# Kernel optimization log

Hardware: AMD Instinct MI355X
Metric: run time of the kernel (lower is better)

The kernel has to match this reference:

```python
import jax, jax.numpy as jnp
import numpy as np

B, T, F = 32, 512, 4096
H = 128            # num_lstm
NUM_CLASSES = 2    # dense outputs = NUM_CLASSES + 1 (CTC blank)


def setup_inputs() -> dict:
    key = jax.random.key(0)
    ks = jax.random.split(key, 6)
    x = jax.random.normal(ks[0], (B, T, F), dtype=jnp.float32)
    # Keras LSTM params: kernel [F, 4H], recurrent_kernel [H, 4H], bias [4H]
    # (gate order i, f, c, o). Glorot-ish scaling for stability.
    Wk = jax.random.normal(ks[1], (F, 4 * H), dtype=jnp.float32) / np.sqrt(F)
    Wr = jax.random.normal(ks[2], (H, 4 * H), dtype=jnp.float32) / np.sqrt(H)
    b = jnp.zeros((4 * H,), dtype=jnp.float32).at[H:2 * H].set(1.0)  # unit_forget_bias
    Wd = jax.random.normal(ks[3], (H, NUM_CLASSES + 1), dtype=jnp.float32) / np.sqrt(H)
    bd = jnp.zeros((NUM_CLASSES + 1,), dtype=jnp.float32)
    return {"x": x, "Wk": Wk, "Wr": Wr, "b": b, "Wd": Wd, "bd": bd}


def _lstm(x, Wk, Wr, b):
    # Precompute input projections for all timesteps (big GEMM once).
    z = jnp.einsum("btf,fg->btg", x, Wk) + b          # [B, T, 4H]
    z = jnp.transpose(z, (1, 0, 2))                    # [T, B, 4H]

    def step(carry, z_t):
        h, c = carry
        g = z_t + h @ Wr                               # [B, 4H]
        i = jax.nn.sigmoid(g[:, 0 * H:1 * H])
        f = jax.nn.sigmoid(g[:, 1 * H:2 * H])
        cc = jnp.tanh(g[:, 2 * H:3 * H])
        o = jax.nn.sigmoid(g[:, 3 * H:4 * H])
        c = f * c + i * cc
        h = o * jnp.tanh(c)
        return (h, c), h

    h0 = jnp.zeros((x.shape[0], H), dtype=x.dtype)
    c0 = jnp.zeros((x.shape[0], H), dtype=x.dtype)
    _, hs = jax.lax.scan(step, (h0, c0), z)            # hs: [T, B, H]
    return jnp.transpose(hs, (1, 0, 2))                # [B, T, H]


def reference(x, Wk, Wr, b, Wd, bd):
    # Inference-mode forward (dropout/recurrent_dropout inactive).
    h = _lstm(x, Wk, Wr, b)                            # [B, T, H]
    return h @ Wd + bd                                 # [B, T, num_classes+1]
```

## Files before the change

kernel.cpp:

```cpp
#include <hip/hip_runtime.h>
#include <hip/hip_bf16.h>
#include <hip/hip_fp16.h>
#include <math.h>

#define B_  32
#define T_  512
#define F_  4096
#define H_  128
#define G4H 512
#define NCLS 3
#define M_  (B_ * T_)
#define KSTEPS 128

typedef _Float16 f16x8 __attribute__((ext_vector_type(8)));
typedef _Float16 f16x4 __attribute__((ext_vector_type(4)));
typedef float    f32x4 __attribute__((ext_vector_type(4)));

__device__ __forceinline__ void gl_lds16(const _Float16* g, _Float16* l) {
    __builtin_amdgcn_global_load_lds(
        (const __attribute__((address_space(1))) void*)(g),
        (__attribute__((address_space(3))) void*)(l), 16, 0, 0);
}

__global__ __launch_bounds__(256) void cvt_wkT(
    const float* __restrict__ Wk, _Float16* __restrict__ btK)
{
    __shared__ float ls[64][65];
    const int k0 = blockIdx.x * 64;
    const int n0 = blockIdx.y * 64;
    const int tid = threadIdx.x;

    {
        int r  = tid >> 4;
        int c4 = (tid & 15) * 4;
        #pragma unroll
        for (int p = 0; p < 4; ++p) {
            float4 v = *reinterpret_cast<const float4*>(
                &Wk[(size_t)(k0 + r + p * 16) * G4H + n0 + c4]);
            ls[r + p * 16][c4 + 0] = v.x;
            ls[r + p * 16][c4 + 1] = v.y;
            ls[r + p * 16][c4 + 2] = v.z;
            ls[r + p * 16][c4 + 3] = v.w;
        }
    }
    __syncthreads();
    {
        int rn = tid >> 2;
        int ck = (tid & 3) * 16;
        f16x8 h0, h1;
        #pragma unroll
        for (int j = 0; j < 8; ++j) {
            h0[j] = (_Float16)ls[ck + j][rn];
            h1[j] = (_Float16)ls[ck + 8 + j][rn];
        }
        const int n    = n0 + rn;
        const int kg   = k0 + ck;
        const int kblk = kg >> 5;
        const int kk   = kg & 31;
        const int g0   = kk >> 3;
        const int sw   = (n >> 1) & 3;
        _Float16* base = btK + (size_t)kblk * (512 * 32) + (size_t)n * 32;
        *reinterpret_cast<f16x8*>(base + ((g0 ^ sw) << 3))       = h0;
        *reinterpret_cast<f16x8*>(base + (((g0 + 1) ^ sw) << 3)) = h1;
    }
}

__global__ __launch_bounds__(256) void cvt_wrT(
    const float* __restrict__ Wr, _Float16* __restrict__ wrT)
{
    __shared__ float ls[64][65];
    const int k0 = blockIdx.x * 64;
    const int n0 = blockIdx.y * 64;
    const int tid = threadIdx.x;
    {
        int r  = tid >> 4;
        int c4 = (tid & 15) * 4;
        #pragma unroll
        for (int p = 0; p < 4; ++p) {
            float4 v = *reinterpret_cast<const float4*>(
                &Wr[(size_t)(k0 + r + p * 16) * G4H + n0 + c4]);
            ls[r + p * 16][c4 + 0] = v.x;
            ls[r + p * 16][c4 + 1] = v.y;
            ls[r + p * 16][c4 + 2] = v.z;
            ls[r + p * 16][c4 + 3] = v.w;
        }
    }
    __syncthreads();
    {
        int rn = tid >> 2;
        int ck = (tid & 3) * 16;
        f16x8 h0, h1;
        #pragma unroll
        for (int j = 0; j < 8; ++j) {
            h0[j] = (_Float16)ls[ck + j][rn];
            h1[j] = (_Float16)ls[ck + 8 + j][rn];
        }
        _Float16* dst = &wrT[(size_t)(n0 + rn) * H_ + k0 + ck];
        *reinterpret_cast<f16x8*>(dst)     = h0;
        *reinterpret_cast<f16x8*>(dst + 8) = h1;
    }
}

__device__ __forceinline__ void lds_barrier() {
    asm volatile("s_waitcnt lgkmcnt(0)" ::: "memory");
    __builtin_amdgcn_s_barrier();
    asm volatile("" ::: "memory");
}

__global__ __launch_bounds__(512, 4) void gemm_fused(
    const float* __restrict__ x, const _Float16* __restrict__ btK,
    const float* __restrict__ bias, float* __restrict__ z)
{
    __shared__ __align__(16) _Float16 As[3][64 * 32];
    __shared__ __align__(16) _Float16 Bs[3][256 * 32];

    const int tid = threadIdx.x;
    const int w   = tid >> 6;
    const int l   = tid & 63;
    const int fr  = l & 15;
    const int q   = l >> 4;

    const int bid   = blockIdx.x;
    const int xcd   = bid & 7;
    const int idx   = bid >> 3;
    const int mt    = xcd * 32 + (idx >> 1);
    const int ntile = idx & 1;
    const int m0    = mt * 64;
    const int n0    = ntile * 256;

    const int ar = tid >> 3;
    const int hc = (tid & 7) * 4;
    const int abyte = ((((hc >> 3) ^ ((ar >> 1) & 3)) << 4) | ((hc << 1) & 15));
    const float* xrow = x + (size_t)(m0 + ar) * F_ + hc;

    #define ISSUE_B(t, buf)                                                   \
    {                                                                         \
        const _Float16* ck_ = btK + (size_t)(t) * (512 * 32) + n0 * 32;       \
        gl_lds16(ck_ + w * 1024 + l * 8,       &Bs[buf][w * 1024]);           \
        gl_lds16(ck_ + w * 1024 + 512 + l * 8, &Bs[buf][w * 1024 + 512]);     \
    }

    #define LOADX(t) (*reinterpret_cast<const float4*>(xrow + (size_t)(t) * 32))

    #define WRITE_A(v, buf)                                                   \
    {                                                                         \
        f16x4 hh; hh[0] = (_Float16)v.x; hh[1] = (_Float16)v.y;               \
        hh[2] = (_Float16)v.z; hh[3] = (_Float16)v.w;                         \
        *reinterpret_cast<f16x4*>(                                            \
            reinterpret_cast<char*>(&As[buf][0]) + ar * 64 + abyte) = hh;     \
    }

    #define COMPUTE(buf)                                                      \
    {                                                                         \
        f16x8 af[4], bf[2];                                                   \
        _Pragma("unroll")                                                     \
        for (int i = 0; i < 4; ++i) {                                         \
            int r   = i * 16 + fr;                                            \
            int off = r * 64 + ((q ^ ((r >> 1) & 3)) << 4);                   \
            af[i] = *reinterpret_cast<const f16x8*>(                          \
                reinterpret_cast<const char*>(&As[buf][0]) + off);            \
        }                                                                     \
        _Pragma("unroll")                                                     \
        for (int j = 0; j < 2; ++j) {                                         \
            int n   = w * 32 + j * 16 + fr;                                   \
            int off = n * 64 + ((q ^ ((n >> 1) & 3)) << 4);                   \
            bf[j] = *reinterpret_cast<const f16x8*>(                          \
                reinterpret_cast<const char*>(&Bs[buf][0]) + off);            \
        }                                                                     \
        _Pragma("unroll")                                                     \
        for (int i = 0; i < 4; ++i)                                           \
            _Pragma("unroll")                                                 \
            for (int j = 0; j < 2; ++j)                                       \
                acc[i][j] = __builtin_amdgcn_mfma_f32_16x16x32_f16(           \
                    af[i], bf[j], acc[i][j], 0, 0, 0);                        \
    }

    f32x4 acc[4][2] = {};
    float4 xvA, xvB;

    ISSUE_B(0, 0) xvA = LOADX(0);
    ISSUE_B(1, 1) xvB = LOADX(1);
    WRITE_A(xvA, 0)
    lds_barrier();

    int b0 = 0, b1 = 1, b2 = 2;
    for (int t = 0; t < KSTEPS; t += 2) {
        if (t + 2 < KSTEPS) { ISSUE_B(t + 2, b2) xvA = LOADX(t + 2); }
        if (t + 1 < KSTEPS) WRITE_A(xvB, b1)
        COMPUTE(b0)
        lds_barrier();
        if (t + 3 < KSTEPS) { ISSUE_B(t + 3, b0) xvB = LOADX(t + 3); }
        if (t + 2 < KSTEPS) WRITE_A(xvA, b2)
        COMPUTE(b1)
        lds_barrier();
        int tmp = b2; b2 = b1; b1 = b0; b0 = tmp;
    }
    #undef ISSUE_B
    #undef LOADX
    #undef WRITE_A
    #undef COMPUTE

    #pragma unroll
    for (int j = 0; j < 2; ++j) {
        const int nn = n0 + w * 32 + j * 16 + fr;
        const int ch = (nn & 127) * 4 + (nn >> 7);
        const float bj = bias[nn];
        #pragma unroll
        for (int i = 0; i < 4; ++i)
            #pragma unroll
            for (int r = 0; r < 4; ++r)
                z[(size_t)(m0 + i * 16 + q * 4 + r) * G4H + ch]
                    = acc[i][j][r] + bj;
    }
}

__device__ __forceinline__ float sig_f(float x) {
    return __builtin_amdgcn_rcpf(
        1.0f + __builtin_amdgcn_exp2f(-1.442695040888963f * x));
}
__device__ __forceinline__ float tanh_f(float x) {
    return 1.0f - 2.0f * __builtin_amdgcn_rcpf(
        1.0f + __builtin_amdgcn_exp2f(2.885390081777927f * x));
}

__global__ __launch_bounds__(512, 2) void lstm_mfma(
    const float* __restrict__ z,
    const _Float16* __restrict__ wrT,
    float* __restrict__ hs)
{
    const int b    = blockIdx.x;
    const int tid  = threadIdx.x;
    const int w    = tid >> 6;
    const int lane = tid & 63;
    const int l15  = lane & 15;
    const int q    = lane >> 4;
    const int jj   = w * 16 + l15;

    __shared__ __align__(16) _Float16 hA[2][128];

    f16x8 bf[4][4];
    #pragma unroll
    for (int g = 0; g < 4; ++g)
        #pragma unroll
        for (int kf = 0; kf < 4; ++kf)
            bf[g][kf] = *reinterpret_cast<const f16x8*>(
                &wrT[(size_t)(g * H_ + jj) * H_ + kf * 32 + q * 8]);

    float cstate = 0.f;
    if (tid < 128) reinterpret_cast<unsigned int*>(hA)[tid] = 0u;

    const float* zrow  = z  + (size_t)b * T_ * G4H + jj * 4;
    float*       hbase = hs + (size_t)b * T_ * H_;

    const f32x4 zero4 = {0.f, 0.f, 0.f, 0.f};

    float4 zP0 = *reinterpret_cast<const float4*>(zrow + (size_t)(0 << 9));
    float4 zP1 = *reinterpret_cast<const float4*>(zrow + (size_t)(1 << 9));
    float4 zP2 = *reinterpret_cast<const float4*>(zrow + (size_t)(2 << 9));
    float4 zP3 = *reinterpret_cast<const float4*>(zrow + (size_t)(3 << 9));

    __syncthreads();

    #define LSTM_STEP(t, CUR, ZZ)                                             \
    {                                                                         \
        f16x8 af0 = *reinterpret_cast<const f16x8*>(&hA[CUR][0 * 32 + q * 8]);\
        f16x8 af1 = *reinterpret_cast<const f16x8*>(&hA[CUR][1 * 32 + q * 8]);\
        f16x8 af2 = *reinterpret_cast<const f16x8*>(&hA[CUR][2 * 32 + q * 8]);\
        f16x8 af3 = *reinterpret_cast<const f16x8*>(&hA[CUR][3 * 32 + q * 8]);\
        float zt0_ = ZZ.x, zt1_ = ZZ.y, zt2_ = ZZ.z, zt3_ = ZZ.w;             \
        ZZ = *reinterpret_cast<const float4*>(                                \
            zrow + (size_t)((((t) + 4) & (T_ - 1)) << 9));                    \
        float gv[4];                                                          \
        _Pragma("unroll")                                                     \
        for (int g = 0; g < 4; ++g) {                                         \
            f32x4 aA = __builtin_amdgcn_mfma_f32_16x16x32_f16(                \
                af0, bf[g][0], zero4, 0, 0, 0);                               \
            aA = __builtin_amdgcn_mfma_f32_16x16x32_f16(                      \
                af1, bf[g][1], aA, 0, 0, 0);                                  \
            f32x4 aB = __builtin_amdgcn_mfma_f32_16x16x32_f16(                \
                af2, bf[g][2], zero4, 0, 0, 0);                               \
            aB = __builtin_amdgcn_mfma_f32_16x16x32_f16(                      \
                af3, bf[g][3], aB, 0, 0, 0);                                  \
            gv[g] = aA[0] + aB[0];                                           \
        }                                                                     \
        float iv = sig_f(gv[0] + zt0_);                                       \
        float fv = sig_f(gv[1] + zt1_);                                       \
        float cc = tanh_f(gv[2] + zt2_);                                      \
        float ov = sig_f(gv[3] + zt3_);                                       \
        cstate = fv * cstate + iv * cc;                                       \
        float h = ov * tanh_f(cstate);                                        \
        if (q == 0) {                                                         \
            hA[CUR ^ 1][jj] = (_Float16)h;                                    \
            hbase[((t) << 7) + jj] = h;                                       \
        }                                                                     \
        lds_barrier();                                                        \
    }

    for (int t = 0; t < T_; t += 4) {
        LSTM_STEP(t,     0, zP0)
        LSTM_STEP(t + 1, 1, zP1)
        LSTM_STEP(t + 2, 0, zP2)
        LSTM_STEP(t + 3, 1, zP3)
    }
    #undef LSTM_STEP
}

__global__ __launch_bounds__(256) void dense_out(
    const float* __restrict__ hs, const float* __restrict__ Wd,
    const float* __restrict__ bd, float* __restrict__ out)
{
    int idx = blockIdx.x * 256 + threadIdx.x;
    if (idx >= B_ * T_ * NCLS) return;
    int cls = idx % NCLS;
    int row = idx / NCLS;
    const float* h = hs + (size_t)row * H_;
    float acc = bd[cls];
    #pragma unroll 8
    for (int k = 0; k < H_; ++k) acc += h[k] * Wd[k * NCLS + cls];
    out[idx] = acc;
}

extern "C" void kernel_launch(void* const* d_in, const int* in_sizes, int n_in,
                              void* d_out, int out_size, void* d_ws, size_t ws_size,
                              hipStream_t stream)
{
    const float* x  = (const float*)d_in[0];
    const float* Wk = (const float*)d_in[1];
    const float* Wr = (const float*)d_in[2];
    const float* b  = (const float*)d_in[3];
    const float* Wd = (const float*)d_in[4];
    const float* bd = (const float*)d_in[5];
    float* out = (float*)d_out;

    float*     z   = (float*)d_ws;
    float*     hs  = z + (size_t)M_ * G4H;
    _Float16*  btK = (_Float16*)(hs + (size_t)M_ * H_);
    _Float16*  wrT = btK + (size_t)G4H * F_;

    cvt_wkT<<<dim3(F_ / 64, G4H / 64), 256, 0, stream>>>(Wk, btK);
    cvt_wrT<<<dim3(H_ / 64, G4H / 64), 256, 0, stream>>>(Wr, wrT);
    gemm_fused<<<512, 512, 0, stream>>>(x, btK, b, z);
    lstm_mfma<<<B_, 512, 0, stream>>>(z, wrT, hs);
    int total = B_ * T_ * NCLS;
    dense_out<<<(total + 255) / 256, 256, 0, stream>>>(hs, Wd, bd, out);
}
```

Baseline: 368.9 us.

## Fuse input GEMM and LSTM recurrence with flag-based per-chunk overlap

Merges the input-projection GEMM and the LSTM recurrence into one persistent launch. The first 32 blocks run the recurrence, one per batch row, and the remaining 512 blocks compute GEMM tiles. Tiles are reordered by batch and time chunk, and each one signals completion through an atomic flag, so the recurrence for a batch row can start as soon as its first 64-step chunk of z is ready. This overlaps the sequential recurrence with the GEMM and removes a kernel boundary. In exchange it relies on spin-waiting with cross-block memory ordering, assumes all blocks become resident without deadlock, and increases LDS use per block, which may lower GEMM occupancy.

```diff
diff --git a/kernel.cpp b/kernel.cpp
--- a/kernel.cpp
+++ b/kernel.cpp
@@ -66,12 +66,14 @@
 }
 
 __global__ __launch_bounds__(256) void cvt_wrT(
-    const float* __restrict__ Wr, _Float16* __restrict__ wrT)
+    const float* __restrict__ Wr, _Float16* __restrict__ wrT,
+    unsigned int* __restrict__ flags)
 {
     __shared__ float ls[64][65];
     const int k0 = blockIdx.x * 64;
     const int n0 = blockIdx.y * 64;
     const int tid = threadIdx.x;
+    if (blockIdx.x == 0 && blockIdx.y == 0) flags[tid] = 0u;
     {
         int r  = tid >> 4;
         int c4 = (tid & 15) * 4;
@@ -107,113 +109,6 @@
     asm volatile("" ::: "memory");
 }
 
-__global__ __launch_bounds__(512, 4) void gemm_fused(
-    const float* __restrict__ x, const _Float16* __restrict__ btK,
-    const float* __restrict__ bias, float* __restrict__ z)
-{
-    __shared__ __align__(16) _Float16 As[3][64 * 32];
-    __shared__ __align__(16) _Float16 Bs[3][256 * 32];
-
-    const int tid = threadIdx.x;
-    const int w   = tid >> 6;
-    const int l   = tid & 63;
-    const int fr  = l & 15;
-    const int q   = l >> 4;
-
-    const int bid   = blockIdx.x;
-    const int xcd   = bid & 7;
-    const int idx   = bid >> 3;
-    const int mt    = xcd * 32 + (idx >> 1);
-    const int ntile = idx & 1;
-    const int m0    = mt * 64;
-    const int n0    = ntile * 256;
-
-    const int ar = tid >> 3;
-    const int hc = (tid & 7) * 4;
-    const int abyte = ((((hc >> 3) ^ ((ar >> 1) & 3)) << 4) | ((hc << 1) & 15));
-    const float* xrow = x + (size_t)(m0 + ar) * F_ + hc;
-
-    #define ISSUE_B(t, buf)                                                   \
-    {                                                                         \
-        const _Float16* ck_ = btK + (size_t)(t) * (512 * 32) + n0 * 32;       \
-        gl_lds16(ck_ + w * 1024 + l * 8,       &Bs[buf][w * 1024]);           \
-        gl_lds16(ck_ + w * 1024 + 512 + l * 8, &Bs[buf][w * 1024 + 512]);     \
-    }
-
-    #define LOADX(t) (*reinterpret_cast<const float4*>(xrow + (size_t)(t) * 32))
-
-    #define WRITE_A(v, buf)                                                   \
-    {                                                                         \
-        f16x4 hh; hh[0] = (_Float16)v.x; hh[1] = (_Float16)v.y;               \
-        hh[2] = (_Float16)v.z; hh[3] = (_Float16)v.w;                         \
-        *reinterpret_cast<f16x4*>(                                            \
-            reinterpret_cast<char*>(&As[buf][0]) + ar * 64 + abyte) = hh;     \
-    }
-
-    #define COMPUTE(buf)                                                      \
-    {                                                                         \
-        f16x8 af[4], bf[2];                                                   \
-        _Pragma("unroll")                                                     \
-        for (int i = 0; i < 4; ++i) {                                         \
-            int r   = i * 16 + fr;                                            \
-            int off = r * 64 + ((q ^ ((r >> 1) & 3)) << 4);                   \
-            af[i] = *reinterpret_cast<const f16x8*>(                          \
-                reinterpret_cast<const char*>(&As[buf][0]) + off);            \
-        }                                                                     \
-        _Pragma("unroll")                                                     \
-        for (int j = 0; j < 2; ++j) {                                         \
-            int n   = w * 32 + j * 16 + fr;                                   \
-            int off = n * 64 + ((q ^ ((n >> 1) & 3)) << 4);                   \
-            bf[j] = *reinterpret_cast<const f16x8*>(                          \
-                reinterpret_cast<const char*>(&Bs[buf][0]) + off);            \
-        }                                                                     \
-        _Pragma("unroll")                                                     \
-        for (int i = 0; i < 4; ++i)                                           \
-            _Pragma("unroll")                                                 \
-            for (int j = 0; j < 2; ++j)                                       \
-                acc[i][j] = __builtin_amdgcn_mfma_f32_16x16x32_f16(           \
-                    af[i], bf[j], acc[i][j], 0, 0, 0);                        \
-    }
-
-    f32x4 acc[4][2] = {};
-    float4 xvA, xvB;
-
-    ISSUE_B(0, 0) xvA = LOADX(0);
-    ISSUE_B(1, 1) xvB = LOADX(1);
-    WRITE_A(xvA, 0)
-    lds_barrier();
-
-    int b0 = 0, b1 = 1, b2 = 2;
-    for (int t = 0; t < KSTEPS; t += 2) {
-        if (t + 2 < KSTEPS) { ISSUE_B(t + 2, b2) xvA = LOADX(t + 2); }
-        if (t + 1 < KSTEPS) WRITE_A(xvB, b1)
-        COMPUTE(b0)
-        lds_barrier();
-        if (t + 3 < KSTEPS) { ISSUE_B(t + 3, b0) xvB = LOADX(t + 3); }
-        if (t + 2 < KSTEPS) WRITE_A(xvA, b2)
-        COMPUTE(b1)
-        lds_barrier();
-        int tmp = b2; b2 = b1; b1 = b0; b0 = tmp;
-    }
-    #undef ISSUE_B
-    #undef LOADX
-    #undef WRITE_A
-    #undef COMPUTE
-
-    #pragma unroll
-    for (int j = 0; j < 2; ++j) {
-        const int nn = n0 + w * 32 + j * 16 + fr;
-        const int ch = (nn & 127) * 4 + (nn >> 7);
-        const float bj = bias[nn];
-        #pragma unroll
-        for (int i = 0; i < 4; ++i)
-            #pragma unroll
-            for (int r = 0; r < 4; ++r)
-                z[(size_t)(m0 + i * 16 + q * 4 + r) * G4H + ch]
-                    = acc[i][j][r] + bj;
-    }
-}
-
 __device__ __forceinline__ float sig_f(float x) {
     return __builtin_amdgcn_rcpf(
         1.0f + __builtin_amdgcn_exp2f(-1.442695040888963f * x));
@@ -223,86 +118,218 @@
         1.0f + __builtin_amdgcn_exp2f(2.885390081777927f * x));
 }
 
-__global__ __launch_bounds__(512, 2) void lstm_mfma(
-    const float* __restrict__ z,
-    const _Float16* __restrict__ wrT,
-    float* __restrict__ hs)
-{
-    const int b    = blockIdx.x;
-    const int tid  = threadIdx.x;
-    const int w    = tid >> 6;
-    const int lane = tid & 63;
-    const int l15  = lane & 15;
-    const int q    = lane >> 4;
-    const int jj   = w * 16 + l15;
-
-    __shared__ __align__(16) _Float16 hA[2][128];
-
-    f16x8 bf[4][4];
-    #pragma unroll
-    for (int g = 0; g < 4; ++g)
-        #pragma unroll
-        for (int kf = 0; kf < 4; ++kf)
-            bf[g][kf] = *reinterpret_cast<const f16x8*>(
-                &wrT[(size_t)(g * H_ + jj) * H_ + kf * 32 + q * 8]);
-
-    float cstate = 0.f;
-    if (tid < 128) reinterpret_cast<unsigned int*>(hA)[tid] = 0u;
-
-    const float* zrow  = z  + (size_t)b * T_ * G4H + jj * 4;
-    float*       hbase = hs + (size_t)b * T_ * H_;
-
-    const f32x4 zero4 = {0.f, 0.f, 0.f, 0.f};
-
-    float4 zP0 = *reinterpret_cast<const float4*>(zrow + (size_t)(0 << 9));
-    float4 zP1 = *reinterpret_cast<const float4*>(zrow + (size_t)(1 << 9));
-    float4 zP2 = *reinterpret_cast<const float4*>(zrow + (size_t)(2 << 9));
-    float4 zP3 = *reinterpret_cast<const float4*>(zrow + (size_t)(3 << 9));
-
-    __syncthreads();
-
-    #define LSTM_STEP(t, CUR, ZZ)                                             \
-    {                                                                         \
-        f16x8 af0 = *reinterpret_cast<const f16x8*>(&hA[CUR][0 * 32 + q * 8]);\
-        f16x8 af1 = *reinterpret_cast<const f16x8*>(&hA[CUR][1 * 32 + q * 8]);\
-        f16x8 af2 = *reinterpret_cast<const f16x8*>(&hA[CUR][2 * 32 + q * 8]);\
-        f16x8 af3 = *reinterpret_cast<const f16x8*>(&hA[CUR][3 * 32 + q * 8]);\
-        float zt0_ = ZZ.x, zt1_ = ZZ.y, zt2_ = ZZ.z, zt3_ = ZZ.w;             \
-        ZZ = *reinterpret_cast<const float4*>(                                \
-            zrow + (size_t)((((t) + 4) & (T_ - 1)) << 9));                    \
-        float gv[4];                                                          \
-        _Pragma("unroll")                                                     \
-        for (int g = 0; g < 4; ++g) {                                         \
-            f32x4 aA = __builtin_amdgcn_mfma_f32_16x16x32_f16(                \
-                af0, bf[g][0], zero4, 0, 0, 0);                               \
-            aA = __builtin_amdgcn_mfma_f32_16x16x32_f16(                      \
-                af1, bf[g][1], aA, 0, 0, 0);                                  \
-            f32x4 aB = __builtin_amdgcn_mfma_f32_16x16x32_f16(                \
-                af2, bf[g][2], zero4, 0, 0, 0);                               \
-            aB = __builtin_amdgcn_mfma_f32_16x16x32_f16(                      \
-                af3, bf[g][3], aB, 0, 0, 0);                                  \
-            gv[g] = aA[0] + aB[0];                                           \
-        }                                                                     \
-        float iv = sig_f(gv[0] + zt0_);                                       \
-        float fv = sig_f(gv[1] + zt1_);                                       \
-        float cc = tanh_f(gv[2] + zt2_);                                      \
-        float ov = sig_f(gv[3] + zt3_);                                       \
-        cstate = fv * cstate + iv * cc;                                       \
-        float h = ov * tanh_f(cstate);                                        \
-        if (q == 0) {                                                         \
-            hA[CUR ^ 1][jj] = (_Float16)h;                                    \
-            hbase[((t) << 7) + jj] = h;                                       \
-        }                                                                     \
-        lds_barrier();                                                        \
-    }
-
-    for (int t = 0; t < T_; t += 4) {
-        LSTM_STEP(t,     0, zP0)
-        LSTM_STEP(t + 1, 1, zP1)
-        LSTM_STEP(t + 2, 0, zP2)
-        LSTM_STEP(t + 3, 1, zP3)
-    }
-    #undef LSTM_STEP
+__device__ __forceinline__ void wait_flag2(unsigned int* f) {
+    while (__hip_atomic_load(f, __ATOMIC_ACQUIRE, __HIP_MEMORY_SCOPE_AGENT) < 2u)
+        __builtin_amdgcn_s_sleep(2);
+}
+
+__global__ __launch_bounds__(512, 2) void fused_gemm_lstm(
+    const float* __restrict__ x, const _Float16* __restrict__ btK,
+    const float* __restrict__ bias, float* __restrict__ z,
+    const _Float16* __restrict__ wrT, float* __restrict__ hs,
+    unsigned int* __restrict__ flags)
+{
+    __shared__ __align__(16) char smem[61440];
+    const int bid = blockIdx.x;
+    const int tid = threadIdx.x;
+
+    if (bid >= B_) {
+        char* AsB = smem;
+        char* BsB = smem + 12288;
+
+        const int w   = tid >> 6;
+        const int l   = tid & 63;
+        const int fr  = l & 15;
+        const int q   = l >> 4;
+
+        const int gbid  = bid - B_;
+        const int s     = gbid >> 6;
+        const int i6    = gbid & 63;
+        const int xx    = i6 & 7;
+        const int yy    = (i6 >> 4) & 3;
+        const int ntile = (i6 >> 3) & 1;
+        const int bb    = xx * 4 + yy;
+        const int m0    = bb * T_ + s * 64;
+        const int n0    = ntile * 256;
+
+        const int ar = tid >> 3;
+        const int hc = (tid & 7) * 4;
+        const int abyte = ((((hc >> 3) ^ ((ar >> 1) & 3)) << 4) | ((hc << 1) & 15));
+        const float* xrow = x + (size_t)(m0 + ar) * F_ + hc;
+
+        #define ISSUE_B(t, buf)                                               \
+        {                                                                     \
+            const _Float16* ck_ = btK + (size_t)(t) * (512 * 32) + n0 * 32;   \
+            _Float16* bb_ = (_Float16*)(BsB + (buf) * 16384) + w * 1024;      \
+            gl_lds16(ck_ + w * 1024 + l * 8,       bb_);                      \
+            gl_lds16(ck_ + w * 1024 + 512 + l * 8, bb_ + 512);                \
+        }
+
+        #define LOADX(t) (*reinterpret_cast<const float4*>(xrow + (size_t)(t) * 32))
+
+        #define WRITE_A(v, buf)                                               \
+        {                                                                     \
+            f16x4 hh; hh[0] = (_Float16)v.x; hh[1] = (_Float16)v.y;           \
+            hh[2] = (_Float16)v.z; hh[3] = (_Float16)v.w;                     \
+            *reinterpret_cast<f16x4*>(                                        \
+                AsB + (buf) * 4096 + ar * 64 + abyte) = hh;                   \
+        }
+
+        #define COMPUTE(buf)                                                  \
+        {                                                                     \
+            f16x8 af[4], bf[2];                                               \
+            _Pragma("unroll")                                                 \
+            for (int i = 0; i < 4; ++i) {                                     \
+                int r   = i * 16 + fr;                                        \
+                int off = r * 64 + ((q ^ ((r >> 1) & 3)) << 4);               \
+                af[i] = *reinterpret_cast<const f16x8*>(                      \
+                    AsB + (buf) * 4096 + off);                                \
+            }                                                                 \
+            _Pragma("unroll")                                                 \
+            for (int j = 0; j < 2; ++j) {                                     \
+                int n   = w * 32 + j * 16 + fr;                               \
+                int off = n * 64 + ((q ^ ((n >> 1) & 3)) << 4);               \
+                bf[j] = *reinterpret_cast<const f16x8*>(                      \
+                    BsB + (buf) * 16384 + off);                               \
+            }                                                                 \
+            _Pragma("unroll")                                                 \
+            for (int i = 0; i < 4; ++i)                                       \
+                _Pragma("unroll")                                             \
+                for (int j = 0; j < 2; ++j)                                   \
+                    acc[i][j] = __builtin_amdgcn_mfma_f32_16x16x32_f16(       \
+                        af[i], bf[j], acc[i][j], 0, 0, 0);                    \
+        }
+
+        f32x4 acc[4][2] = {};
+        float4 xvA, xvB;
+
+        ISSUE_B(0, 0) xvA = LOADX(0);
+        ISSUE_B(1, 1) xvB = LOADX(1);
+        WRITE_A(xvA, 0)
+        lds_barrier();
+
+        int b0 = 0, b1 = 1, b2 = 2;
+        for (int t = 0; t < KSTEPS; t += 2) {
+            if (t + 2 < KSTEPS) { ISSUE_B(t + 2, b2) xvA = LOADX(t + 2); }
+            if (t + 1 < KSTEPS) WRITE_A(xvB, b1)
+            COMPUTE(b0)
+            lds_barrier();
+            if (t + 3 < KSTEPS) { ISSUE_B(t + 3, b0) xvB = LOADX(t + 3); }
+            if (t + 2 < KSTEPS) WRITE_A(xvA, b2)
+            COMPUTE(b1)
+            lds_barrier();
+            int tmp = b2; b2 = b1; b1 = b0; b0 = tmp;
+        }
+        #undef ISSUE_B
+        #undef LOADX
+        #undef WRITE_A
+        #undef COMPUTE
+
+        #pragma unroll
+        for (int j = 0; j < 2; ++j) {
+            const int nn = n0 + w * 32 + j * 16 + fr;
+            const int ch = (nn & 127) * 4 + (nn >> 7);
+            const float bj = bias[nn];
+            #pragma unroll
+            for (int i = 0; i < 4; ++i)
+                #pragma unroll
+                for (int r = 0; r < 4; ++r)
+                    z[(size_t)(m0 + i * 16 + q * 4 + r) * G4H + ch]
+                        = acc[i][j][r] + bj;
+        }
+
+        __threadfence();
+        __syncthreads();
+        if (tid == 0)
+            __hip_atomic_fetch_add(&flags[(bb << 3) + s], 1u,
+                                   __ATOMIC_RELEASE, __HIP_MEMORY_SCOPE_AGENT);
+        return;
+    }
+
+    {
+        const int b    = bid;
+        const int w    = tid >> 6;
+        const int lane = tid & 63;
+        const int l15  = lane & 15;
+        const int q    = lane >> 4;
+        const int jj   = w * 16 + l15;
+
+        _Float16 (*hA)[128] = reinterpret_cast<_Float16(*)[128]>(smem);
+
+        f16x8 bf[4][4];
+        #pragma unroll
+        for (int g = 0; g < 4; ++g)
+            #pragma unroll
+            for (int kf = 0; kf < 4; ++kf)
+                bf[g][kf] = *reinterpret_cast<const f16x8*>(
+                    &wrT[(size_t)(g * H_ + jj) * H_ + kf * 32 + q * 8]);
+
+        float cstate = 0.f;
+        if (tid < 128) reinterpret_cast<unsigned int*>(hA)[tid] = 0u;
+
+        const float* zrow  = z  + (size_t)b * T_ * G4H + jj * 4;
+        float*       hbase = hs + (size_t)b * T_ * H_;
+
+        const f32x4 zero4 = {0.f, 0.f, 0.f, 0.f};
+
+        if (tid == 0) wait_flag2(&flags[b << 3]);
+        __syncthreads();
+
+        float4 zP0 = *reinterpret_cast<const float4*>(zrow + (size_t)(0 << 9));
+        float4 zP1 = *reinterpret_cast<const float4*>(zrow + (size_t)(1 << 9));
+        float4 zP2 = *reinterpret_cast<const float4*>(zrow + (size_t)(2 << 9));
+        float4 zP3 = *reinterpret_cast<const float4*>(zrow + (size_t)(3 << 9));
+
+        #define LSTM_STEP(t, CUR, ZZ)                                         \
+        {                                                                     \
+            f16x8 af0 = *reinterpret_cast<const f16x8*>(&hA[CUR][0 * 32 + q * 8]);\
+            f16x8 af1 = *reinterpret_cast<const f16x8*>(&hA[CUR][1 * 32 + q * 8]);\
+            f16x8 af2 = *reinterpret_cast<const f16x8*>(&hA[CUR][2 * 32 + q * 8]);\
+            f16x8 af3 = *reinterpret_cast<const f16x8*>(&hA[CUR][3 * 32 + q * 8]);\
+            float zt0_ = ZZ.x, zt1_ = ZZ.y, zt2_ = ZZ.z, zt3_ = ZZ.w;         \
+            ZZ = *reinterpret_cast<const float4*>(                            \
+                zrow + (size_t)((((t) + 4) & (T_ - 1)) << 9));                \
+            float gv[4];                                                      \
+            _Pragma("unroll")                                                 \
+            for (int g = 0; g < 4; ++g) {                                     \
+                f32x4 aA = __builtin_amdgcn_mfma_f32_16x16x32_f16(            \
+                    af0, bf[g][0], zero4, 0, 0, 0);                           \
+                aA = __builtin_amdgcn_mfma_f32_16x16x32_f16(                  \
+                    af1, bf[g][1], aA, 0, 0, 0);                              \
+                f32x4 aB = __builtin_amdgcn_mfma_f32_16x16x32_f16(            \
+                    af2, bf[g][2], zero4, 0, 0, 0);                           \
+                aB = __builtin_amdgcn_mfma_f32_16x16x32_f16(                  \
+                    af3, bf[g][3], aB, 0, 0, 0);                              \
+                gv[g] = aA[0] + aB[0];                                        \
+            }                                                                 \
+            float iv = sig_f(gv[0] + zt0_);                                   \
+            float fv = sig_f(gv[1] + zt1_);                                   \
+            float cc = tanh_f(gv[2] + zt2_);                                  \
+            float ov = sig_f(gv[3] + zt3_);                                   \
+            cstate = fv * cstate + iv * cc;                                   \
+            float h = ov * tanh_f(cstate);                                    \
+            if (q == 0) {                                                     \
+                hA[CUR ^ 1][jj] = (_Float16)h;                                \
+                hbase[((t) << 7) + jj] = h;                                   \
+            }                                                                 \
+            lds_barrier();                                                    \
+        }
+
+        for (int s8 = 0; s8 < 8; ++s8) {
+            if (tid == 0) {
+                wait_flag2(&flags[(b << 3) + s8]);
+                if (s8 < 7) wait_flag2(&flags[(b << 3) + s8 + 1]);
+            }
+            __syncthreads();
+            for (int t = s8 * 64; t < s8 * 64 + 64; t += 4) {
+                LSTM_STEP(t,     0, zP0)
+                LSTM_STEP(t + 1, 1, zP1)
+                LSTM_STEP(t + 2, 0, zP2)
+                LSTM_STEP(t + 3, 1, zP3)
+            }
+        }
+        #undef LSTM_STEP
+    }
 }
 
 __global__ __launch_bounds__(256) void dense_out(
@@ -332,15 +359,15 @@
     const float* bd = (const float*)d_in[5];
     float* out = (float*)d_out;
 
-    float*     z   = (float*)d_ws;
-    float*     hs  = z + (size_t)M_ * G4H;
-    _Float16*  btK = (_Float16*)(hs + (size_t)M_ * H_);
-    _Float16*  wrT = btK + (size_t)G4H * F_;
+    float*        z     = (float*)d_ws;
+    float*        hs    = z + (size_t)M_ * G4H;
+    _Float16*     btK   = (_Float16*)(hs + (size_t)M_ * H_);
+    _Float16*     wrT   = btK + (size_t)G4H * F_;
+    unsigned int* flags = (unsigned int*)(wrT + (size_t)G4H * H_);
 
     cvt_wkT<<<dim3(F_ / 64, G4H / 64), 256, 0, stream>>>(Wk, btK);
-    cvt_wrT<<<dim3(H_ / 64, G4H / 64), 256, 0, stream>>>(Wr, wrT);
-    gemm_fused<<<512, 512, 0, stream>>>(x, btK, b, z);
-    lstm_mfma<<<B_, 512, 0, stream>>>(z, wrT, hs);
+    cvt_wrT<<<dim3(H_ / 64, G4H / 64), 256, 0, stream>>>(Wr, wrT, flags);
+    fused_gemm_lstm<<<B_ + 512, 512, 0, stream>>>(x, btK, b, z, wrT, hs, flags);
     int total = B_ * T_ * NCLS;
     dense_out<<<(total + 255) / 256, 256, 0, stream>>>(hs, Wd, bd, out);
 }
```

New measurement: 638.7 us. 1.73x slower.

## Deepen X prefetch to four stages with explicit vmcnt waits in GEMM

Applied to the files above, without the earlier changes.

Restructures the input-projection GEMM main loop so X register loads are prefetched four K-steps ahead using a rotating set of four float4 registers. The generic LDS barrier is replaced by hand-placed s_waitcnt vmcnt(N)/lgkmcnt(0) plus s_barrier, so outstanding global loads can stay in flight across the barrier. The aim is to hide global memory latency for the large x tile stream. It adds register pressure and relies on exact counts of outstanding loads, which is fragile if the load instruction count per step changes.

```diff
diff --git a/kernel.cpp b/kernel.cpp
--- a/kernel.cpp
+++ b/kernel.cpp
@@ -175,30 +175,83 @@
                     af[i], bf[j], acc[i][j], 0, 0, 0);                        \
     }
 
+    #define FENCE asm volatile("" ::: "memory");
+
+    #define HALF_ITER(t, XW, XL, VMN)                                         \
+    {                                                                         \
+        ISSUE_B((t) + 2, b2)                                                  \
+        FENCE                                                                 \
+        XL = LOADX((t) + 4);                                                  \
+        FENCE                                                                 \
+        WRITE_A(XW, b1)                                                       \
+        COMPUTE(b0)                                                           \
+        asm volatile("s_waitcnt vmcnt(" #VMN ") lgkmcnt(0)" ::: "memory");    \
+        __builtin_amdgcn_s_barrier();                                         \
+        FENCE                                                                 \
+        int _tmp = b0; b0 = b1; b1 = b2; b2 = _tmp;                           \
+    }
+
     f32x4 acc[4][2] = {};
-    float4 xvA, xvB;
-
-    ISSUE_B(0, 0) xvA = LOADX(0);
-    ISSUE_B(1, 1) xvB = LOADX(1);
-    WRITE_A(xvA, 0)
-    lds_barrier();
-
+    float4 xq0, xq1, xq2, xq3;
     int b0 = 0, b1 = 1, b2 = 2;
-    for (int t = 0; t < KSTEPS; t += 2) {
-        if (t + 2 < KSTEPS) { ISSUE_B(t + 2, b2) xvA = LOADX(t + 2); }
-        if (t + 1 < KSTEPS) WRITE_A(xvB, b1)
+
+    xq0 = LOADX(0);
+    FENCE
+    ISSUE_B(0, 0) ISSUE_B(1, 1)
+    FENCE
+    xq1 = LOADX(1); xq2 = LOADX(2); xq3 = LOADX(3);
+    FENCE
+    WRITE_A(xq0, 0)
+    asm volatile("s_waitcnt vmcnt(5) lgkmcnt(0)" ::: "memory");
+    __builtin_amdgcn_s_barrier();
+    FENCE
+
+    HALF_ITER(0, xq1, xq0, 6)
+
+    for (int t = 1; t <= 117; t += 4) {
+        HALF_ITER(t,     xq2, xq1, 4)
+        HALF_ITER(t + 1, xq3, xq2, 4)
+        HALF_ITER(t + 2, xq0, xq3, 4)
+        HALF_ITER(t + 3, xq1, xq0, 4)
+    }
+    HALF_ITER(121, xq2, xq1, 4)
+    HALF_ITER(122, xq3, xq2, 4)
+    HALF_ITER(123, xq0, xq3, 4)
+
+    {
+        ISSUE_B(126, b2)
+        WRITE_A(xq1, b1)
         COMPUTE(b0)
-        lds_barrier();
-        if (t + 3 < KSTEPS) { ISSUE_B(t + 3, b0) xvB = LOADX(t + 3); }
-        if (t + 2 < KSTEPS) WRITE_A(xvA, b2)
-        COMPUTE(b1)
-        lds_barrier();
-        int tmp = b2; b2 = b1; b1 = b0; b0 = tmp;
-    }
+        asm volatile("s_waitcnt vmcnt(0) lgkmcnt(0)" ::: "memory");
+        __builtin_amdgcn_s_barrier();
+        FENCE
+        int _t = b0; b0 = b1; b1 = b2; b2 = _t;
+    }
+    {
+        ISSUE_B(127, b2)
+        WRITE_A(xq2, b1)
+        COMPUTE(b0)
+        asm volatile("s_waitcnt vmcnt(0) lgkmcnt(0)" ::: "memory");
+        __builtin_amdgcn_s_barrier();
+        FENCE
+        int _t = b0; b0 = b1; b1 = b2; b2 = _t;
+    }
+    {
+        WRITE_A(xq3, b1)
+        COMPUTE(b0)
+        asm volatile("s_waitcnt vmcnt(0) lgkmcnt(0)" ::: "memory");
+        __builtin_amdgcn_s_barrier();
+        FENCE
+        int _t = b0; b0 = b1; b1 = b2; b2 = _t;
+    }
+    COMPUTE(b0)
+
     #undef ISSUE_B
     #undef LOADX
     #undef WRITE_A
     #undef COMPUTE
+    #undef HALF_ITER
+    #undef FENCE
 
     #pragma unroll
     for (int j = 0; j < 2; ++j) {
```

New measurement: 378.1 us. 2.5% more time.

## Load GEMM B fragments directly from global into registers, drop LDS staging

Applied to the files above, without the earlier changes.

The input-projection GEMM no longer stages the fp16 weight tiles through LDS with global_load_lds. Each lane now loads its own swizzled B fragments straight into registers, double-buffered across k-steps, and the LDS triple buffer for A becomes a double buffer. This removes B's LDS traffic and frees LDS, at the cost of more global/L2 loads, since B is no longer shared across the block's waves (each wave reads distinct columns anyway). It also raises register pressure and exposes load latency within the 2-step register pipeline.

```diff
diff --git a/kernel.cpp b/kernel.cpp
--- a/kernel.cpp
+++ b/kernel.cpp
@@ -15,12 +15,6 @@
 typedef _Float16 f16x8 __attribute__((ext_vector_type(8)));
 typedef _Float16 f16x4 __attribute__((ext_vector_type(4)));
 typedef float    f32x4 __attribute__((ext_vector_type(4)));
-
-__device__ __forceinline__ void gl_lds16(const _Float16* g, _Float16* l) {
-    __builtin_amdgcn_global_load_lds(
-        (const __attribute__((address_space(1))) void*)(g),
-        (__attribute__((address_space(3))) void*)(l), 16, 0, 0);
-}
 
 __global__ __launch_bounds__(256) void cvt_wkT(
     const float* __restrict__ Wk, _Float16* __restrict__ btK)
@@ -111,8 +105,7 @@
     const float* __restrict__ x, const _Float16* __restrict__ btK,
     const float* __restrict__ bias, float* __restrict__ z)
 {
-    __shared__ __align__(16) _Float16 As[3][64 * 32];
-    __shared__ __align__(16) _Float16 Bs[3][256 * 32];
+    __shared__ __align__(16) _Float16 As[2][64 * 32];
 
     const int tid = threadIdx.x;
     const int w   = tid >> 6;
@@ -133,11 +126,15 @@
     const int abyte = ((((hc >> 3) ^ ((ar >> 1) & 3)) << 4) | ((hc << 1) & 15));
     const float* xrow = x + (size_t)(m0 + ar) * F_ + hc;
 
-    #define ISSUE_B(t, buf)                                                   \
+    const int nA = n0 + w * 32 + fr;
+    const int nB = nA + 16;
+    const _Float16* bp0 = btK + (size_t)nA * 32 + ((q ^ ((nA >> 1) & 3)) << 3);
+    const _Float16* bp1 = btK + (size_t)nB * 32 + ((q ^ ((nB >> 1) & 3)) << 3);
+
+    #define LOADB(t, bfv)                                                     \
     {                                                                         \
-        const _Float16* ck_ = btK + (size_t)(t) * (512 * 32) + n0 * 32;       \
-        gl_lds16(ck_ + w * 1024 + l * 8,       &Bs[buf][w * 1024]);           \
-        gl_lds16(ck_ + w * 1024 + 512 + l * 8, &Bs[buf][w * 1024 + 512]);     \
+        bfv[0] = *reinterpret_cast<const f16x8*>(bp0 + (size_t)(t) * 16384);  \
+        bfv[1] = *reinterpret_cast<const f16x8*>(bp1 + (size_t)(t) * 16384);  \
     }
 
     #define LOADX(t) (*reinterpret_cast<const float4*>(xrow + (size_t)(t) * 32))
@@ -150,9 +147,9 @@
             reinterpret_cast<char*>(&As[buf][0]) + ar * 64 + abyte) = hh;     \
     }
 
-    #define COMPUTE(buf)                                                      \
+    #define COMPUTE(buf, bfv)                                                 \
     {                                                                         \
-        f16x8 af[4], bf[2];                                                   \
+        f16x8 af[4];                                                          \
         _Pragma("unroll")                                                     \
         for (int i = 0; i < 4; ++i) {                                         \
             int r   = i * 16 + fr;                                            \
@@ -161,41 +158,40 @@
                 reinterpret_cast<const char*>(&As[buf][0]) + off);            \
         }                                                                     \
         _Pragma("unroll")                                                     \
-        for (int j = 0; j < 2; ++j) {                                         \
-            int n   = w * 32 + j * 16 + fr;                                   \
-            int off = n * 64 + ((q ^ ((n >> 1) & 3)) << 4);                   \
-            bf[j] = *reinterpret_cast<const f16x8*>(                          \
-                reinterpret_cast<const char*>(&Bs[buf][0]) + off);            \
-        }                                                                     \
-        _Pragma("unroll")                                                     \
         for (int i = 0; i < 4; ++i)                                           \
             _Pragma("unroll")                                                 \
             for (int j = 0; j < 2; ++j)                                       \
                 acc[i][j] = __builtin_amdgcn_mfma_f32_16x16x32_f16(           \
-                    af[i], bf[j], acc[i][j], 0, 0, 0);                        \
+                    af[i], bfv[j], acc[i][j], 0, 0, 0);                       \
     }
 
     f32x4 acc[4][2] = {};
-    float4 xvA, xvB;
-
-    ISSUE_B(0, 0) xvA = LOADX(0);
-    ISSUE_B(1, 1) xvB = LOADX(1);
-    WRITE_A(xvA, 0)
+    f16x8 bfA[2], bfB[2];
+    float4 xa, xb;
+
+    xa = LOADX(0); xb = LOADX(1);
+    LOADB(0, bfA) LOADB(1, bfB)
+    WRITE_A(xa, 0)
     lds_barrier();
 
-    int b0 = 0, b1 = 1, b2 = 2;
-    for (int t = 0; t < KSTEPS; t += 2) {
-        if (t + 2 < KSTEPS) { ISSUE_B(t + 2, b2) xvA = LOADX(t + 2); }
-        if (t + 1 < KSTEPS) WRITE_A(xvB, b1)
-        COMPUTE(b0)
+    for (int t = 0; t < 126; t += 2) {
+        xa = LOADX(t + 2);
+        WRITE_A(xb, 1)
+        COMPUTE(0, bfA)
+        LOADB(t + 2, bfA)
         lds_barrier();
-        if (t + 3 < KSTEPS) { ISSUE_B(t + 3, b0) xvB = LOADX(t + 3); }
-        if (t + 2 < KSTEPS) WRITE_A(xvA, b2)
-        COMPUTE(b1)
+        xb = LOADX(t + 3);
+        WRITE_A(xa, 0)
+        COMPUTE(1, bfB)
+        LOADB(t + 3, bfB)
         lds_barrier();
-        int tmp = b2; b2 = b1; b1 = b0; b0 = tmp;
-    }
-    #undef ISSUE_B
+    }
+    WRITE_A(xb, 1)
+    COMPUTE(0, bfA)
+    lds_barrier();
+    COMPUTE(1, bfB)
+
+    #undef LOADB
     #undef LOADX
     #undef WRITE_A
     #undef COMPUTE
```

Measured after the change: 375.0 us. About the same (+1.7%).
